# Kernel optimization log

Hardware: AMD Instinct MI355X
Metric: run time of the kernel (lower is better)

## Reference

```python
import jax, jax.numpy as jnp
import numpy as np

# Module config (matches init_kwargs)
N_HEADS = 16
HEAD = 64
SEQ = 4096          # single prefill sequence (cu_seqlens_k = [0, SEQ])
BS = 64             # block_size (both q and k blocks)
LOCAL = 8           # local_blocks
VERT = 8            # vert_stride
NB = SEQ // BS      # number of blocks along seq
SLIDE = max(1, VERT // N_HEADS)  # get_head_sliding_step(16, 8, homo_head=False) -> 1
SM_SCALE = 1.0 / float(np.sqrt(HEAD))


def _build_layout():
    """Per-head block-sparse layout: causal + (local OR strided-vertical) blocks,
    padded to a fixed max nnz per row (CSR rows -> padded col indices + valid mask)."""
    h = np.arange(N_HEADS)[:, None, None]
    i = np.arange(NB)[None, :, None]
    j = np.arange(NB)[None, None, :]
    mask = (j <= i) & (((i - j) < LOCAL) | (((j + h * SLIDE + 1) % VERT) == 0))
    max_nnz = int(mask.sum(-1).max())
    cols = np.zeros((N_HEADS, NB, max_nnz), np.int32)
    valid = np.zeros((N_HEADS, NB, max_nnz), bool)
    for hh in range(N_HEADS):
        for ii in range(NB):
            c = np.nonzero(mask[hh, ii])[0]
            cols[hh, ii, :len(c)] = c
            valid[hh, ii, :len(c)] = True
    return cols, valid, max_nnz

_COLS_NP, _VALID_NP, MAX_NNZ = _build_layout()
COLS = jnp.asarray(_COLS_NP)    # [H, NB, NNZ] k-block ids (padded with 0)
VALID = jnp.asarray(_VALID_NP)  # [H, NB, NNZ] padding mask


def setup_inputs() -> dict:
    key = jax.random.key(0)
    kq, kk, kv = jax.random.split(key, 3)
    q = jax.random.normal(kq, (SEQ, N_HEADS, HEAD), jnp.float32)
    k = jax.random.normal(kk, (SEQ, N_HEADS, HEAD), jnp.float32)
    v = jax.random.normal(kv, (SEQ, N_HEADS, HEAD), jnp.float32)
    cu_seqlens_k = jnp.array([0, SEQ], jnp.int32)
    return {"q": q, "k": k, "v": v, "cu_seqlens_k": cu_seqlens_k}


def _attn(q, k, v):
    # [T, H, D] -> [H, NB, BS, D]
    qb = q.transpose(1, 0, 2).reshape(N_HEADS, NB, BS, HEAD)
    kb = k.transpose(1, 0, 2).reshape(N_HEADS, NB, BS, HEAD)
    vb = v.transpose(1, 0, 2).reshape(N_HEADS, NB, BS, HEAD)
    gather = jax.vmap(lambda x, c: x[c])  # per-head block gather
    kg = gather(kb, COLS)  # [H, NB, NNZ, BS, D]
    vg = gather(vb, COLS)  # [H, NB, NNZ, BS, D]
    # block-sparse scores: [H, NB(q blk), BS(m), NNZ(n), BS(j)]
    scores = jnp.einsum('himd,hinjd->himnj', qb, kg) * SM_SCALE
    qpos = jnp.arange(NB)[:, None] * BS + jnp.arange(BS)[None, :]   # [NB, BS]
    kpos = COLS[..., None] * BS + jnp.arange(BS)                    # [H, NB, NNZ, BS]
    allow = VALID[:, :, None, :, None] & (
        qpos[None, :, :, None, None] >= kpos[:, :, None, :, :])
    scores = jnp.where(allow, scores, -jnp.inf)
    p = jax.nn.softmax(scores.reshape(N_HEADS, NB, BS, MAX_NNZ * BS), axis=-1)
    p = p.reshape(N_HEADS, NB, BS, MAX_NNZ, BS)
    out = jnp.einsum('himnj,hinjd->himd', p, vg)
    return out.reshape(N_HEADS, SEQ, HEAD).transpose(1, 0, 2)  # [T, H, D]


def reference(q, k, v, cu_seqlens_k):
    # single-sequence prefill: past_len = 0, q_len == k_len == SEQ
    return _attn(q, k, v)
```

## Files before the change

kernel.cpp:

```cpp
#include <hip/hip_runtime.h>
#include <hip/hip_bf16.h>
#include <math.h>


#define NHEADS 16
#define HDIM   64
#define NBLK   64
#define SEQLEN 4096
#define KP     72
#define SMAX   16.0f
#define NEGBIG (-1.0e30f)

typedef __attribute__((ext_vector_type(8))) short bf16x8;
typedef __attribute__((ext_vector_type(4))) float f32x4;

__device__ __forceinline__ short f2bf(float x) {
    union { float f; unsigned u; } c; c.f = x;
    unsigned u = c.u;
    return (short)((u + 0x7FFFu + ((u >> 16) & 1u)) >> 16);
}
__device__ __forceinline__ short f2bf_trunc(float x) {
    union { float f; unsigned u; } c; c.f = x;
    return (short)(c.u >> 16);
}

__device__ __forceinline__ void load_lds16(const short* g, const short* l) {
    __builtin_amdgcn_global_load_lds(
        (const __attribute__((address_space(1))) void*)g,
        (__attribute__((address_space(3))) void*)l, 16, 0, 0);
}

__device__ __forceinline__ void drain_then_sync() {
    asm volatile("s_waitcnt vmcnt(0)" ::: "memory");
    __syncthreads();
}

__global__ __launch_bounds__(256)
void prep_kernel(const float* __restrict__ k, const float* __restrict__ v,
                 short* __restrict__ kt, short* __restrict__ vt) {
    __shared__ short tile[64 * KP];
    const int b = blockIdx.x;
    const int h = b >> 6, jb = b & 63;
    const int tid = threadIdx.x;

    #pragma unroll
    for (int it = 0; it < 4; ++it) {
        int e = it * 1024 + tid * 4;
        int key = e >> 6, d0 = e & 63;
        float4 f = *(const float4*)(v + ((size_t)(jb * 64 + key) * NHEADS + h) * HDIM + d0);
        tile[(d0 + 0) * KP + key] = f2bf(f.x);
        tile[(d0 + 1) * KP + key] = f2bf(f.y);
        tile[(d0 + 2) * KP + key] = f2bf(f.z);
        tile[(d0 + 3) * KP + key] = f2bf(f.w);
    }
    __syncthreads();
    short* vtile = vt + (size_t)b * 4096;
    #pragma unroll
    for (int ii = 0; ii < 2; ++ii) {
        int idx = ii * 256 + tid;
        int d = idx >> 3, gsw = idx & 7;
        int g = gsw ^ (d & 7);
        bf16x8 val;
        #pragma unroll
        for (int j = 0; j < 8; ++j) {
            int s   = g * 8 + j;
            int key = (s & 32) | (((s >> 2) & 1) << 4) | (((s >> 3) & 3) << 2) | (s & 3);
            val[j]  = tile[d * KP + key];
        }
        *(bf16x8*)(vtile + (size_t)idx * 8) = val;
    }
    short* ktile = kt + (size_t)b * 4096;
    #pragma unroll
    for (int ii = 0; ii < 2; ++ii) {
        int idx = ii * 256 + tid;
        int r = idx >> 3, g = idx & 7;
        const float* src = k + ((size_t)(jb * 64 + r) * NHEADS + h) * HDIM + g * 8;
        float4 f0 = *(const float4*)src;
        float4 f1 = *(const float4*)(src + 4);
        bf16x8 a;
        a[0]=f2bf(f0.x); a[1]=f2bf(f0.y); a[2]=f2bf(f0.z); a[3]=f2bf(f0.w);
        a[4]=f2bf(f1.x); a[5]=f2bf(f1.y); a[6]=f2bf(f1.z); a[7]=f2bf(f1.w);
        int G = r * 8 + (g ^ (r & 7));
        *(bf16x8*)(ktile + (size_t)G * 8) = a;
    }
}

__global__ __launch_bounds__(512, 4)
void attn_kernel(const short* __restrict__ kt, const short* __restrict__ vt,
                 const float* __restrict__ q, float* __restrict__ out) {
    __shared__ short kv[2 * 8192];

    const int b    = blockIdx.x;
    const int h    = ((b & 7) << 1) | ((b >> 3) & 1);
    const int g5   = b >> 4;
    const int m    = (g5 < 16) ? g5 : (47 - g5);
    const int q0   = 2 * m, q1 = 2 * m + 1;
    const int tid  = threadIdx.x;
    const int wave = tid >> 6;
    const int lane = tid & 63;
    const int l16  = lane & 15;
    const int quad = lane >> 4;

    const int myqi   = q0 + (wave >> 2);
    const int stripe = wave & 3;
    const int row0   = myqi * 64 + stripe * 16;

    const float* qrow = q + ((size_t)(row0 + l16) * NHEADS + h) * HDIM;
    bf16x8 a_q[2];
    #pragma unroll
    for (int kk = 0; kk < 2; ++kk) {
        const float* src = qrow + kk * 32 + quad * 8;
        float4 f0 = *(const float4*)(src);
        float4 f1 = *(const float4*)(src + 4);
        bf16x8 a;
        a[0]=f2bf(f0.x); a[1]=f2bf(f0.y); a[2]=f2bf(f0.z); a[3]=f2bf(f0.w);
        a[4]=f2bf(f1.x); a[5]=f2bf(f1.y); a[6]=f2bf(f1.z); a[7]=f2bf(f1.w);
        a_q[kk] = a;
    }

    f32x4 o[4];
    #pragma unroll
    for (int nt = 0; nt < 4; ++nt) o[nt] = (f32x4){0.f,0.f,0.f,0.f};
    float lsum = 0.f;

    const short* kth = kt + (size_t)(h * 64) * 4096;
    const short* vth = vt + (size_t)(h * 64) * 4096;
    const float kscale = 0.125f * 1.4426950408889634f;

    const int j0  = (7 - h) & 7;
    const int l0  = (q0 > 7) ? (q0 - 7) : 0;
    const int nv  = (j0 < l0) ? ((l0 - j0 + 7) >> 3) : 0;
    const int T   = nv + (q1 - l0 + 1);

    const int r7   = l16 & 7;
    const int gk0  = (quad ^ r7) * 8;
    const int gk1  = gk0 ^ 32;
    const int rowb = l16 * 64;
    const int qrl  = stripe * 16 + l16;

    {
        const short* ktb = kth + (size_t)((0 < nv) ? j0 : l0) * 4096;
        const short* vtb = vth + (size_t)((0 < nv) ? j0 : l0) * 4096;
        load_lds16(ktb + (size_t)tid * 8, &kv[wave * 512]);
        load_lds16(vtb + (size_t)tid * 8, &kv[4096 + wave * 512]);
    }

    for (int t = 0; t < T; ++t) {
        const int jb = (t < nv) ? (j0 + 8 * t) : (l0 + (t - nv));

        drain_then_sync();

        if (t + 1 < T) {
            const int jn = (t + 1 < nv) ? (j0 + 8 * (t + 1)) : (l0 + (t + 1 - nv));
            const int bo = ((t + 1) & 1) * 8192;
            const short* ktb = kth + (size_t)jn * 4096;
            const short* vtb = vth + (size_t)jn * 4096;
            load_lds16(ktb + (size_t)tid * 8, &kv[bo + wave * 512]);
            load_lds16(vtb + (size_t)tid * 8, &kv[bo + 4096 + wave * 512]);
        }

        const bool part = (jb <= myqi) &&
                          (((myqi - jb) < 8) || (((jb + h + 1) & 7) == 0));
        if (part) {
            const short* kb = &kv[(t & 1) * 8192];
            const short* vb = kb + 4096;
            const bool diag = (jb == myqi);

            f32x4 s[4];
            #pragma unroll
            for (int nt = 0; nt < 4; ++nt) {
                bf16x8 k0 = *(const bf16x8*)&kb[nt * 1024 + rowb + gk0];
                bf16x8 k1 = *(const bf16x8*)&kb[nt * 1024 + rowb + gk1];
                f32x4 acc = (f32x4){0.f, 0.f, 0.f, 0.f};
                acc = __builtin_amdgcn_mfma_f32_16x16x32_bf16(k0, a_q[0], acc, 0, 0, 0);
                acc = __builtin_amdgcn_mfma_f32_16x16x32_bf16(k1, a_q[1], acc, 0, 0, 0);
                s[nt] = acc;
            }

            short pb[4][4];
            #pragma unroll
            for (int nt = 0; nt < 4; ++nt) {
                #pragma unroll
                for (int r = 0; r < 4; ++r) {
                    const int keyl = nt * 16 + quad * 4 + r;
                    float raw = s[nt][r];
                    raw = (diag && (keyl > qrl)) ? NEGBIG : raw;
                    float pv = __builtin_amdgcn_exp2f(fmaf(raw, kscale, -SMAX));
                    lsum += pv;
                    pb[nt][r] = f2bf_trunc(pv);
                }
            }

            bf16x8 a_p0, a_p1;
            a_p0[0]=pb[0][0]; a_p0[1]=pb[0][1]; a_p0[2]=pb[0][2]; a_p0[3]=pb[0][3];
            a_p0[4]=pb[1][0]; a_p0[5]=pb[1][1]; a_p0[6]=pb[1][2]; a_p0[7]=pb[1][3];
            a_p1[0]=pb[2][0]; a_p1[1]=pb[2][1]; a_p1[2]=pb[2][2]; a_p1[3]=pb[2][3];
            a_p1[4]=pb[3][0]; a_p1[5]=pb[3][1]; a_p1[6]=pb[3][2]; a_p1[7]=pb[3][3];

            #pragma unroll
            for (int nt = 0; nt < 4; ++nt) {
                bf16x8 v0 = *(const bf16x8*)&vb[nt * 1024 + rowb + gk0];
                bf16x8 v1 = *(const bf16x8*)&vb[nt * 1024 + rowb + gk1];
                o[nt] = __builtin_amdgcn_mfma_f32_16x16x32_bf16(a_p0, v0, o[nt], 0, 0, 0);
                o[nt] = __builtin_amdgcn_mfma_f32_16x16x32_bf16(a_p1, v1, o[nt], 0, 0, 0);
            }
        }
    }

    float tsum = lsum;
    tsum += __shfl_xor(tsum, 16);
    tsum += __shfl_xor(tsum, 32);
    const float inv = 1.0f / tsum;
    #pragma unroll
    for (int r = 0; r < 4; ++r) {
        float invr = __shfl(inv, quad * 4 + r);
        int trow = row0 + quad * 4 + r;
        float* orow = out + ((size_t)trow * NHEADS + h) * HDIM;
        #pragma unroll
        for (int nt = 0; nt < 4; ++nt)
            orow[nt * 16 + l16] = o[nt][r] * invr;
    }
}

extern "C" void kernel_launch(void* const* d_in, const int* in_sizes, int n_in,
                              void* d_out, int out_size, void* d_ws, size_t ws_size,
                              hipStream_t stream) {
    const float* q = (const float*)d_in[0];
    const float* k = (const float*)d_in[1];
    const float* v = (const float*)d_in[2];
    float* out = (float*)d_out;

    const size_t tileBytes = (size_t)NHEADS * NBLK * 4096 * sizeof(short);
    short* kt = (short*)d_ws;
    short* vt = (short*)((char*)d_ws + tileBytes);
    prep_kernel<<<dim3(NHEADS * NBLK), dim3(256), 0, stream>>>(k, v, kt, vt);
    attn_kernel<<<dim3(512), dim3(512), 0, stream>>>(kt, vt, q, out);
}
```

Before: 114.6 us.

## Drop LDS staging and load K/V fragments directly from global per query block

```diff
diff --git a/kernel.cpp b/kernel.cpp
--- a/kernel.cpp
+++ b/kernel.cpp
@@ -22,17 +22,6 @@
 __device__ __forceinline__ short f2bf_trunc(float x) {
     union { float f; unsigned u; } c; c.f = x;
     return (short)(c.u >> 16);
-}
-
-__device__ __forceinline__ void load_lds16(const short* g, const short* l) {
-    __builtin_amdgcn_global_load_lds(
-        (const __attribute__((address_space(1))) void*)g,
-        (__attribute__((address_space(3))) void*)l, 16, 0, 0);
-}
-
-__device__ __forceinline__ void drain_then_sync() {
-    asm volatile("s_waitcnt vmcnt(0)" ::: "memory");
-    __syncthreads();
 }
 
 __global__ __launch_bounds__(256)
@@ -85,25 +74,20 @@
     }
 }
 
-__global__ __launch_bounds__(512, 4)
+__global__ __launch_bounds__(256)
 void attn_kernel(const short* __restrict__ kt, const short* __restrict__ vt,
                  const float* __restrict__ q, float* __restrict__ out) {
-    __shared__ short kv[2 * 8192];
-
     const int b    = blockIdx.x;
     const int h    = ((b & 7) << 1) | ((b >> 3) & 1);
-    const int g5   = b >> 4;
-    const int m    = (g5 < 16) ? g5 : (47 - g5);
-    const int q0   = 2 * m, q1 = 2 * m + 1;
+    const int m    = b >> 4;
+    const int qi   = (m & 1) ? (63 - (m >> 1)) : (m >> 1);
     const int tid  = threadIdx.x;
-    const int wave = tid >> 6;
+    const int stripe = tid >> 6;
     const int lane = tid & 63;
     const int l16  = lane & 15;
     const int quad = lane >> 4;
 
-    const int myqi   = q0 + (wave >> 2);
-    const int stripe = wave & 3;
-    const int row0   = myqi * 64 + stripe * 16;
+    const int row0 = qi * 64 + stripe * 16;
 
     const float* qrow = q + ((size_t)(row0 + l16) * NHEADS + h) * HDIM;
     bf16x8 a_q[2];
@@ -128,82 +112,77 @@
     const float kscale = 0.125f * 1.4426950408889634f;
 
     const int j0  = (7 - h) & 7;
-    const int l0  = (q0 > 7) ? (q0 - 7) : 0;
+    const int l0  = (qi > 7) ? (qi - 7) : 0;
     const int nv  = (j0 < l0) ? ((l0 - j0 + 7) >> 3) : 0;
-    const int T   = nv + (q1 - l0 + 1);
+    const int T   = nv + (qi - l0 + 1);
 
     const int r7   = l16 & 7;
-    const int gk0  = (quad ^ r7) * 8;
-    const int gk1  = gk0 ^ 32;
-    const int rowb = l16 * 64;
+    const int off0 = l16 * 64 + (quad ^ r7) * 8;
+    const int off1 = off0 ^ 32;
     const int qrl  = stripe * 16 + l16;
-
-    {
-        const short* ktb = kth + (size_t)((0 < nv) ? j0 : l0) * 4096;
-        const short* vtb = vth + (size_t)((0 < nv) ? j0 : l0) * 4096;
-        load_lds16(ktb + (size_t)tid * 8, &kv[wave * 512]);
-        load_lds16(vtb + (size_t)tid * 8, &kv[4096 + wave * 512]);
-    }
 
     for (int t = 0; t < T; ++t) {
         const int jb = (t < nv) ? (j0 + 8 * t) : (l0 + (t - nv));
-
-        drain_then_sync();
-
-        if (t + 1 < T) {
-            const int jn = (t + 1 < nv) ? (j0 + 8 * (t + 1)) : (l0 + (t + 1 - nv));
-            const int bo = ((t + 1) & 1) * 8192;
-            const short* ktb = kth + (size_t)jn * 4096;
-            const short* vtb = vth + (size_t)jn * 4096;
-            load_lds16(ktb + (size_t)tid * 8, &kv[bo + wave * 512]);
-            load_lds16(vtb + (size_t)tid * 8, &kv[bo + 4096 + wave * 512]);
-        }
-
-        const bool part = (jb <= myqi) &&
-                          (((myqi - jb) < 8) || (((jb + h + 1) & 7) == 0));
-        if (part) {
-            const short* kb = &kv[(t & 1) * 8192];
-            const short* vb = kb + 4096;
-            const bool diag = (jb == myqi);
-
-            f32x4 s[4];
-            #pragma unroll
-            for (int nt = 0; nt < 4; ++nt) {
-                bf16x8 k0 = *(const bf16x8*)&kb[nt * 1024 + rowb + gk0];
-                bf16x8 k1 = *(const bf16x8*)&kb[nt * 1024 + rowb + gk1];
-                f32x4 acc = (f32x4){0.f, 0.f, 0.f, 0.f};
-                acc = __builtin_amdgcn_mfma_f32_16x16x32_bf16(k0, a_q[0], acc, 0, 0, 0);
-                acc = __builtin_amdgcn_mfma_f32_16x16x32_bf16(k1, a_q[1], acc, 0, 0, 0);
-                s[nt] = acc;
-            }
-
-            short pb[4][4];
-            #pragma unroll
-            for (int nt = 0; nt < 4; ++nt) {
+        const short* kb = kth + (size_t)jb * 4096;
+        const short* vb = vth + (size_t)jb * 4096;
+        const bool diag = (jb == qi);
+
+        bf16x8 kf0[4], kf1[4];
+        #pragma unroll
+        for (int nt = 0; nt < 4; ++nt) {
+            kf0[nt] = *(const bf16x8*)&kb[nt * 1024 + off0];
+            kf1[nt] = *(const bf16x8*)&kb[nt * 1024 + off1];
+        }
+
+        f32x4 s[4];
+        #pragma unroll
+        for (int nt = 0; nt < 4; ++nt) {
+            f32x4 acc = (f32x4){0.f, 0.f, 0.f, 0.f};
+            acc = __builtin_amdgcn_mfma_f32_16x16x32_bf16(kf0[nt], a_q[0], acc, 0, 0, 0);
+            acc = __builtin_amdgcn_mfma_f32_16x16x32_bf16(kf1[nt], a_q[1], acc, 0, 0, 0);
+            s[nt] = acc;
+        }
+
+        bf16x8 vf0[4], vf1[4];
+        #pragma unroll
+        for (int nt = 0; nt < 4; ++nt) {
+            vf0[nt] = *(const bf16x8*)&vb[nt * 1024 + off0];
+            vf1[nt] = *(const bf16x8*)&vb[nt * 1024 + off1];
+        }
+
+        short pb[4][4];
+        float ls[4];
+        #pragma unroll
+        for (int nt = 0; nt < 4; ++nt) {
+            float l01, l23;
+            {
+                float pv0, pv1, pv2, pv3;
                 #pragma unroll
                 for (int r = 0; r < 4; ++r) {
                     const int keyl = nt * 16 + quad * 4 + r;
                     float raw = s[nt][r];
                     raw = (diag && (keyl > qrl)) ? NEGBIG : raw;
                     float pv = __builtin_amdgcn_exp2f(fmaf(raw, kscale, -SMAX));
-                    lsum += pv;
                     pb[nt][r] = f2bf_trunc(pv);
+                    if (r == 0) pv0 = pv; else if (r == 1) pv1 = pv;
+                    else if (r == 2) pv2 = pv; else pv3 = pv;
                 }
+                l01 = pv0 + pv1; l23 = pv2 + pv3;
             }
-
-            bf16x8 a_p0, a_p1;
-            a_p0[0]=pb[0][0]; a_p0[1]=pb[0][1]; a_p0[2]=pb[0][2]; a_p0[3]=pb[0][3];
-            a_p0[4]=pb[1][0]; a_p0[5]=pb[1][1]; a_p0[6]=pb[1][2]; a_p0[7]=pb[1][3];
-            a_p1[0]=pb[2][0]; a_p1[1]=pb[2][1]; a_p1[2]=pb[2][2]; a_p1[3]=pb[2][3];
-            a_p1[4]=pb[3][0]; a_p1[5]=pb[3][1]; a_p1[6]=pb[3][2]; a_p1[7]=pb[3][3];
-
-            #pragma unroll
-            for (int nt = 0; nt < 4; ++nt) {
-                bf16x8 v0 = *(const bf16x8*)&vb[nt * 1024 + rowb + gk0];
-                bf16x8 v1 = *(const bf16x8*)&vb[nt * 1024 + rowb + gk1];
-                o[nt] = __builtin_amdgcn_mfma_f32_16x16x32_bf16(a_p0, v0, o[nt], 0, 0, 0);
-                o[nt] = __builtin_amdgcn_mfma_f32_16x16x32_bf16(a_p1, v1, o[nt], 0, 0, 0);
-            }
+            ls[nt] = l01 + l23;
+        }
+        lsum += (ls[0] + ls[1]) + (ls[2] + ls[3]);
+
+        bf16x8 a_p0, a_p1;
+        a_p0[0]=pb[0][0]; a_p0[1]=pb[0][1]; a_p0[2]=pb[0][2]; a_p0[3]=pb[0][3];
+        a_p0[4]=pb[1][0]; a_p0[5]=pb[1][1]; a_p0[6]=pb[1][2]; a_p0[7]=pb[1][3];
+        a_p1[0]=pb[2][0]; a_p1[1]=pb[2][1]; a_p1[2]=pb[2][2]; a_p1[3]=pb[2][3];
+        a_p1[4]=pb[3][0]; a_p1[5]=pb[3][1]; a_p1[6]=pb[3][2]; a_p1[7]=pb[3][3];
+
+        #pragma unroll
+        for (int nt = 0; nt < 4; ++nt) {
+            o[nt] = __builtin_amdgcn_mfma_f32_16x16x32_bf16(a_p0, vf0[nt], o[nt], 0, 0, 0);
+            o[nt] = __builtin_amdgcn_mfma_f32_16x16x32_bf16(a_p1, vf1[nt], o[nt], 0, 0, 0);
         }
     }
 
@@ -234,5 +213,5 @@
     short* kt = (short*)d_ws;
     short* vt = (short*)((char*)d_ws + tileBytes);
     prep_kernel<<<dim3(NHEADS * NBLK), dim3(256), 0, stream>>>(k, v, kt, vt);
-    attn_kernel<<<dim3(512), dim3(512), 0, stream>>>(kt, vt, q, out);
-}
+    attn_kernel<<<dim3(1024), dim3(256), 0, stream>>>(kt, vt, q, out);
+}
```

Result: slower. 135.7 us (+18.4%).

## Split attention work to one query block per workgroup with interleaved scheduling

Applied to the files above, without the earlier changes.

```diff
diff --git a/kernel.cpp b/kernel.cpp
--- a/kernel.cpp
+++ b/kernel.cpp
@@ -85,25 +85,22 @@
     }
 }
 
-__global__ __launch_bounds__(512, 4)
+__global__ __launch_bounds__(256, 4)
 void attn_kernel(const short* __restrict__ kt, const short* __restrict__ vt,
                  const float* __restrict__ q, float* __restrict__ out) {
     __shared__ short kv[2 * 8192];
 
     const int b    = blockIdx.x;
     const int h    = ((b & 7) << 1) | ((b >> 3) & 1);
-    const int g5   = b >> 4;
-    const int m    = (g5 < 16) ? g5 : (47 - g5);
-    const int q0   = 2 * m, q1 = 2 * m + 1;
+    const int idx  = b >> 4;
+    const int qi   = (idx & 1) ? (63 - (idx >> 1)) : (idx >> 1);
     const int tid  = threadIdx.x;
-    const int wave = tid >> 6;
+    const int stripe = tid >> 6;
     const int lane = tid & 63;
     const int l16  = lane & 15;
     const int quad = lane >> 4;
 
-    const int myqi   = q0 + (wave >> 2);
-    const int stripe = wave & 3;
-    const int row0   = myqi * 64 + stripe * 16;
+    const int row0 = qi * 64 + stripe * 16;
 
     const float* qrow = q + ((size_t)(row0 + l16) * NHEADS + h) * HDIM;
     bf16x8 a_q[2];
@@ -128,9 +125,9 @@
     const float kscale = 0.125f * 1.4426950408889634f;
 
     const int j0  = (7 - h) & 7;
-    const int l0  = (q0 > 7) ? (q0 - 7) : 0;
+    const int l0  = (qi > 7) ? (qi - 7) : 0;
     const int nv  = (j0 < l0) ? ((l0 - j0 + 7) >> 3) : 0;
-    const int T   = nv + (q1 - l0 + 1);
+    const int T   = nv + (qi - l0 + 1);
 
     const int r7   = l16 & 7;
     const int gk0  = (quad ^ r7) * 8;
@@ -139,15 +136,16 @@
     const int qrl  = stripe * 16 + l16;
 
     {
-        const short* ktb = kth + (size_t)((0 < nv) ? j0 : l0) * 4096;
-        const short* vtb = vth + (size_t)((0 < nv) ? j0 : l0) * 4096;
-        load_lds16(ktb + (size_t)tid * 8, &kv[wave * 512]);
-        load_lds16(vtb + (size_t)tid * 8, &kv[4096 + wave * 512]);
+        const int jb0 = (0 < nv) ? j0 : l0;
+        const short* ktb = kth + (size_t)jb0 * 4096;
+        const short* vtb = vth + (size_t)jb0 * 4096;
+        load_lds16(ktb + (size_t)tid * 8,         &kv[stripe * 512]);
+        load_lds16(ktb + (size_t)(tid + 256) * 8, &kv[2048 + stripe * 512]);
+        load_lds16(vtb + (size_t)tid * 8,         &kv[4096 + stripe * 512]);
+        load_lds16(vtb + (size_t)(tid + 256) * 8, &kv[6144 + stripe * 512]);
     }
 
     for (int t = 0; t < T; ++t) {
-        const int jb = (t < nv) ? (j0 + 8 * t) : (l0 + (t - nv));
-
         drain_then_sync();
 
         if (t + 1 < T) {
@@ -155,56 +153,58 @@
             const int bo = ((t + 1) & 1) * 8192;
             const short* ktb = kth + (size_t)jn * 4096;
             const short* vtb = vth + (size_t)jn * 4096;
-            load_lds16(ktb + (size_t)tid * 8, &kv[bo + wave * 512]);
-            load_lds16(vtb + (size_t)tid * 8, &kv[bo + 4096 + wave * 512]);
-        }
-
-        const bool part = (jb <= myqi) &&
-                          (((myqi - jb) < 8) || (((jb + h + 1) & 7) == 0));
-        if (part) {
-            const short* kb = &kv[(t & 1) * 8192];
-            const short* vb = kb + 4096;
-            const bool diag = (jb == myqi);
-
-            f32x4 s[4];
+            load_lds16(ktb + (size_t)tid * 8,         &kv[bo + stripe * 512]);
+            load_lds16(ktb + (size_t)(tid + 256) * 8, &kv[bo + 2048 + stripe * 512]);
+            load_lds16(vtb + (size_t)tid * 8,         &kv[bo + 4096 + stripe * 512]);
+            load_lds16(vtb + (size_t)(tid + 256) * 8, &kv[bo + 6144 + stripe * 512]);
+        }
+
+        const short* kb = &kv[(t & 1) * 8192];
+        const short* vb = kb + 4096;
+        const bool diag = (t == T - 1);
+
+        __builtin_amdgcn_s_setprio(1);
+
+        f32x4 s[4];
+        #pragma unroll
+        for (int nt = 0; nt < 4; ++nt) {
+            bf16x8 k0 = *(const bf16x8*)&kb[nt * 1024 + rowb + gk0];
+            bf16x8 k1 = *(const bf16x8*)&kb[nt * 1024 + rowb + gk1];
+            f32x4 acc = (f32x4){0.f, 0.f, 0.f, 0.f};
+            acc = __builtin_amdgcn_mfma_f32_16x16x32_bf16(k0, a_q[0], acc, 0, 0, 0);
+            acc = __builtin_amdgcn_mfma_f32_16x16x32_bf16(k1, a_q[1], acc, 0, 0, 0);
+            s[nt] = acc;
+        }
+
+        short pb[4][4];
+        #pragma unroll
+        for (int nt = 0; nt < 4; ++nt) {
             #pragma unroll
-            for (int nt = 0; nt < 4; ++nt) {
-                bf16x8 k0 = *(const bf16x8*)&kb[nt * 1024 + rowb + gk0];
-                bf16x8 k1 = *(const bf16x8*)&kb[nt * 1024 + rowb + gk1];
-                f32x4 acc = (f32x4){0.f, 0.f, 0.f, 0.f};
-                acc = __builtin_amdgcn_mfma_f32_16x16x32_bf16(k0, a_q[0], acc, 0, 0, 0);
-                acc = __builtin_amdgcn_mfma_f32_16x16x32_bf16(k1, a_q[1], acc, 0, 0, 0);
-                s[nt] = acc;
+            for (int r = 0; r < 4; ++r) {
+                const int keyl = nt * 16 + quad * 4 + r;
+                float raw = s[nt][r];
+                raw = (diag && (keyl > qrl)) ? NEGBIG : raw;
+                float pv = __builtin_amdgcn_exp2f(fmaf(raw, kscale, -SMAX));
+                lsum += pv;
+                pb[nt][r] = f2bf_trunc(pv);
             }
-
-            short pb[4][4];
-            #pragma unroll
-            for (int nt = 0; nt < 4; ++nt) {
-                #pragma unroll
-                for (int r = 0; r < 4; ++r) {
-                    const int keyl = nt * 16 + quad * 4 + r;
-                    float raw = s[nt][r];
-                    raw = (diag && (keyl > qrl)) ? NEGBIG : raw;
-                    float pv = __builtin_amdgcn_exp2f(fmaf(raw, kscale, -SMAX));
-                    lsum += pv;
-                    pb[nt][r] = f2bf_trunc(pv);
-                }
-            }
-
-            bf16x8 a_p0, a_p1;
-            a_p0[0]=pb[0][0]; a_p0[1]=pb[0][1]; a_p0[2]=pb[0][2]; a_p0[3]=pb[0][3];
-            a_p0[4]=pb[1][0]; a_p0[5]=pb[1][1]; a_p0[6]=pb[1][2]; a_p0[7]=pb[1][3];
-            a_p1[0]=pb[2][0]; a_p1[1]=pb[2][1]; a_p1[2]=pb[2][2]; a_p1[3]=pb[2][3];
-            a_p1[4]=pb[3][0]; a_p1[5]=pb[3][1]; a_p1[6]=pb[3][2]; a_p1[7]=pb[3][3];
-
-            #pragma unroll
-            for (int nt = 0; nt < 4; ++nt) {
-                bf16x8 v0 = *(const bf16x8*)&vb[nt * 1024 + rowb + gk0];
-                bf16x8 v1 = *(const bf16x8*)&vb[nt * 1024 + rowb + gk1];
-                o[nt] = __builtin_amdgcn_mfma_f32_16x16x32_bf16(a_p0, v0, o[nt], 0, 0, 0);
-                o[nt] = __builtin_amdgcn_mfma_f32_16x16x32_bf16(a_p1, v1, o[nt], 0, 0, 0);
-            }
-        }
+        }
+
+        bf16x8 a_p0, a_p1;
+        a_p0[0]=pb[0][0]; a_p0[1]=pb[0][1]; a_p0[2]=pb[0][2]; a_p0[3]=pb[0][3];
+        a_p0[4]=pb[1][0]; a_p0[5]=pb[1][1]; a_p0[6]=pb[1][2]; a_p0[7]=pb[1][3];
+        a_p1[0]=pb[2][0]; a_p1[1]=pb[2][1]; a_p1[2]=pb[2][2]; a_p1[3]=pb[2][3];
+        a_p1[4]=pb[3][0]; a_p1[5]=pb[3][1]; a_p1[6]=pb[3][2]; a_p1[7]=pb[3][3];
+
+        #pragma unroll
+        for (int nt = 0; nt < 4; ++nt) {
+            bf16x8 v0 = *(const bf16x8*)&vb[nt * 1024 + rowb + gk0];
+            bf16x8 v1 = *(const bf16x8*)&vb[nt * 1024 + rowb + gk1];
+            o[nt] = __builtin_amdgcn_mfma_f32_16x16x32_bf16(a_p0, v0, o[nt], 0, 0, 0);
+            o[nt] = __builtin_amdgcn_mfma_f32_16x16x32_bf16(a_p1, v1, o[nt], 0, 0, 0);
+        }
+
+        __builtin_amdgcn_s_setprio(0);
     }
 
     float tsum = lsum;
@@ -234,5 +234,5 @@
     short* kt = (short*)d_ws;
     short* vt = (short*)((char*)d_ws + tileBytes);
     prep_kernel<<<dim3(NHEADS * NBLK), dim3(256), 0, stream>>>(k, v, kt, vt);
-    attn_kernel<<<dim3(512), dim3(512), 0, stream>>>(kt, vt, q, out);
-}
+    attn_kernel<<<dim3(1024), dim3(256), 0, stream>>>(kt, vt, q, out);
+}
```

Result: faster. 111.4 us (-2.8%).
